# Performance work log

Measured on AMD Instinct MI355X. Metric: run time of the kernel, lower is better.

## Reference

```python
import jax, jax.numpy as jnp
import numpy as np

B, H, W, C = 32, 256, 256, 3
FLAT = (H // 4) * (W // 4) * 64  # 64*64*64 = 262144 after two stride-2 SAME convs


def _conv(x, k, b, stride):
    y = jax.lax.conv_general_dilated(
        x, k, (stride, stride), 'SAME',
        dimension_numbers=('NHWC', 'HWIO', 'NHWC'))
    return jax.nn.relu(y + b)


def _grid_sample(img, theta):
    # STN: build normalized affine grid from theta [B,2,3], bilinear sample with
    # zero padding for out-of-bounds (GridSampler2D semantics).
    b, h, w, c = img.shape
    xs = (2.0 * jnp.arange(w, dtype=img.dtype) + 1.0) / w - 1.0
    ys = (2.0 * jnp.arange(h, dtype=img.dtype) + 1.0) / h - 1.0
    X, Y = jnp.meshgrid(xs, ys)                      # [H,W]
    base = jnp.stack([X, Y, jnp.ones_like(X)], -1)   # [H,W,3]
    g = jnp.einsum('bij,hwj->bhwi', theta, base)     # [B,H,W,2] (x,y) in [-1,1]
    px = (g[..., 0] + 1.0) * 0.5 * w - 0.5
    py = (g[..., 1] + 1.0) * 0.5 * h - 0.5
    x0 = jnp.floor(px); y0 = jnp.floor(py)
    wx1 = px - x0; wx0 = 1.0 - wx1
    wy1 = py - y0; wy0 = 1.0 - wy1

    bidx = jnp.arange(b)[:, None, None]

    def gather(yi, xi):
        valid = (xi >= 0) & (xi < w) & (yi >= 0) & (yi < h)
        xc = jnp.clip(xi, 0, w - 1).astype(jnp.int32)
        yc = jnp.clip(yi, 0, h - 1).astype(jnp.int32)
        v = img[bidx, yc, xc]                        # [B,H,W,C]
        return v * valid[..., None].astype(img.dtype)

    out = (gather(y0, x0) * (wy0 * wx0)[..., None]
           + gather(y0, x0 + 1) * (wy0 * wx1)[..., None]
           + gather(y0 + 1, x0) * (wy1 * wx0)[..., None]
           + gather(y0 + 1, x0 + 1) * (wy1 * wx1)[..., None])
    return out


def setup_inputs() -> dict:
    key = jax.random.key(0)
    ks = jax.random.split(key, 9)
    s = 0.05
    return {
        'inputs': jax.random.uniform(ks[0], (B, H, W, C), jnp.float32),
        'k1': jax.random.normal(ks[1], (3, 3, C, 32), jnp.float32) * s,
        'b1': jnp.zeros((32,), jnp.float32),
        'k2': jax.random.normal(ks[2], (3, 3, 32, 64), jnp.float32) * s,
        'b2': jnp.zeros((64,), jnp.float32),
        'w1': jax.random.normal(ks[3], (FLAT, 128), jnp.float32) * 0.002,
        'd1': jnp.zeros((128,), jnp.float32),
        'w2': jax.random.normal(ks[4], (128, 6), jnp.float32) * s,
        'd2': jnp.asarray([1, 0, 0, 0, 1, 0], jnp.float32),  # identity-ish bias
    }


def reference(inputs, k1, b1, k2, b2, w1, d1, w2, d2):
    x = _conv(inputs, k1, b1, 2)          # [B,H/2,W/2,32]
    x = _conv(x, k2, b2, 2)               # [B,H/4,W/4,64]
    x = x.reshape(x.shape[0], -1)         # [B,FLAT]
    x = jax.nn.relu(x @ w1 + d1)          # [B,128]
    theta = (x @ w2 + d2).reshape(-1, 2, 3)
    return _grid_sample(inputs, theta)
```

## Files before the change

kernel.cpp:

```cpp
#include <hip/hip_runtime.h>

#define IN_H 256
#define IN_W 256
#define C0   3
#define C1   32
#define H1   128
#define C2   64
#define H2   64
#define NB   32
#define K_FLAT (H2*H2*C2)
#define NHID 128

#define A1_IDX(b,y,p,ci,x2) (((((size_t)(b)*H1 + (y))*2 + (p))*C1 + (ci))*64 + (x2))

__global__ __launch_bounds__(256)
void conv1_k(const float* __restrict__ in, const float* __restrict__ k1,
             const float* __restrict__ b1, float* __restrict__ a1p) {
  const int tid = threadIdx.x;
  const int ox  = tid & 127;
  const int cg  = __builtin_amdgcn_readfirstlane((tid >> 7) * 16);
  const int oy  = blockIdx.x;
  const int b   = blockIdx.y;

  float acc[16];
#pragma unroll
  for (int co = 0; co < 16; ++co) acc[co] = b1[cg + co];

#pragma unroll
  for (int dy = 0; dy < 3; ++dy) {
    const int iy  = 2*oy + dy;
    const bool rok = iy < IN_H;
    const int iyc = rok ? iy : (IN_H-1);
#pragma unroll
    for (int dx = 0; dx < 3; ++dx) {
      const int ix  = 2*ox + dx;
      const bool ok = rok && (ix < IN_W);
      const int ixc = (ix < IN_W) ? ix : (IN_W-1);
      const float* ip = in + ((size_t)(b*IN_H + iyc)*IN_W + ixc)*C0;
      const float v0 = ok ? ip[0] : 0.f;
      const float v1 = ok ? ip[1] : 0.f;
      const float v2 = ok ? ip[2] : 0.f;
      const float* wp = k1 + (size_t)((dy*3+dx)*C0)*C1 + cg;
#pragma unroll
      for (int co = 0; co < 16; ++co)
        acc[co] = fmaf(v0, wp[co],
                  fmaf(v1, wp[C1+co],
                  fmaf(v2, wp[2*C1+co], acc[co])));
    }
  }
  const int p  = ox & 1;
  const int x2 = ox >> 1;
#pragma unroll
  for (int co = 0; co < 16; ++co)
    a1p[A1_IDX(b, oy, p, cg + co, x2)] = fmaxf(acc[co], 0.f);
}

__global__ __launch_bounds__(256)
void conv2_k(const float* __restrict__ a1p, const float* __restrict__ k2,
             const float* __restrict__ b2, float* __restrict__ a2) {
  const int tid = threadIdx.x;
  const int ox  = tid & 63;
  const int cg16 = __builtin_amdgcn_readfirstlane((tid >> 6) * 16);
  const int oy  = blockIdx.x;
  const int b   = blockIdx.y;

  float acc[16];
#pragma unroll
  for (int co = 0; co < 16; ++co) acc[co] = b2[cg16 + co];

#pragma unroll
  for (int dy = 0; dy < 3; ++dy) {
    const int iy  = 2*oy + dy;
    const bool rok = iy < H1;
    const int iyc = rok ? iy : (H1-1);
#pragma unroll
    for (int dx = 0; dx < 3; ++dx) {
      const int p   = dx & 1;
      const int x2  = ox + (dx >> 1);
      const bool ok = rok && (x2 < 64);
      const int x2c = (x2 < 64) ? x2 : 63;
      const float* ip = a1p + A1_IDX(b, iyc, p, 0, x2c);
      const float* wp = k2 + (size_t)((dy*3+dx)*C1)*C2 + cg16;
#pragma unroll
      for (int ci = 0; ci < C1; ++ci) {
        float v = ip[(size_t)ci*64];
        v = ok ? v : 0.f;
        const float* wr = wp + (size_t)ci*C2;
#pragma unroll
        for (int co = 0; co < 16; ++co) acc[co] = fmaf(v, wr[co], acc[co]);
      }
    }
  }
  float* op = a2 + ((size_t)(b*H2 + oy)*H2 + ox)*C2 + cg16;
#pragma unroll
  for (int g = 0; g < 4; ++g) {
    float4 o;
    o.x = fmaxf(acc[4*g+0], 0.f);
    o.y = fmaxf(acc[4*g+1], 0.f);
    o.z = fmaxf(acc[4*g+2], 0.f);
    o.w = fmaxf(acc[4*g+3], 0.f);
    ((float4*)op)[g] = o;
  }
}

#define FC1_G   1024
#define KSPAN   (K_FLAT / FC1_G)

__global__ __launch_bounds__(256)
void fc1_partial_k(const float* __restrict__ a2, const float* __restrict__ w1,
                   float* __restrict__ partial) {
  __shared__ __align__(16) float xT[KSPAN*36];
  const int tid = threadIdx.x;
  const int q   = tid & 31;
  const int bo  = tid >> 5;
  const int k0  = blockIdx.x * KSPAN;

  {
    const int lb  = tid >> 3;
    const int lkq = tid & 7;
#pragma unroll
    for (int j = 0; j < 8; ++j) {
      const int k4 = lkq*4 + j*32;
      float4 t = *(const float4*)(a2 + (size_t)lb*K_FLAT + k0 + k4);
      xT[(k4+0)*36 + lb] = t.x;
      xT[(k4+1)*36 + lb] = t.y;
      xT[(k4+2)*36 + lb] = t.z;
      xT[(k4+3)*36 + lb] = t.w;
    }
  }
  __syncthreads();

  float4 a0 = make_float4(0.f,0.f,0.f,0.f), a1v = a0, a2v = a0, a3v = a0;
#pragma unroll 4
  for (int k = 0; k < KSPAN; ++k) {
    const float4 w4 = *(const float4*)(w1 + (size_t)(k0 + k)*NHID + 4*q);
    const float4 xb = *(const float4*)&xT[k*36 + 4*bo];
    a0.x = fmaf(xb.x, w4.x, a0.x); a0.y = fmaf(xb.x, w4.y, a0.y);
    a0.z = fmaf(xb.x, w4.z, a0.z); a0.w = fmaf(xb.x, w4.w, a0.w);
    a1v.x = fmaf(xb.y, w4.x, a1v.x); a1v.y = fmaf(xb.y, w4.y, a1v.y);
    a1v.z = fmaf(xb.y, w4.z, a1v.z); a1v.w = fmaf(xb.y, w4.w, a1v.w);
    a2v.x = fmaf(xb.z, w4.x, a2v.x); a2v.y = fmaf(xb.z, w4.y, a2v.y);
    a2v.z = fmaf(xb.z, w4.z, a2v.z); a2v.w = fmaf(xb.z, w4.w, a2v.w);
    a3v.x = fmaf(xb.w, w4.x, a3v.x); a3v.y = fmaf(xb.w, w4.y, a3v.y);
    a3v.z = fmaf(xb.w, w4.z, a3v.z); a3v.w = fmaf(xb.w, w4.w, a3v.w);
  }

  float* pp = partial + (size_t)blockIdx.x*(NB*NHID) + 4*q;
  *(float4*)(pp + (4*bo+0)*NHID) = a0;
  *(float4*)(pp + (4*bo+1)*NHID) = a1v;
  *(float4*)(pp + (4*bo+2)*NHID) = a2v;
  *(float4*)(pp + (4*bo+3)*NHID) = a3v;
}

__global__ __launch_bounds__(128)
void fc1_reduce1_k(const float* __restrict__ partial, float* __restrict__ partial2) {
  const int t  = blockIdx.x*128 + threadIdx.x;
  const int gc = blockIdx.y;
  float s = 0.f;
#pragma unroll 8
  for (int g = gc*128; g < gc*128+128; ++g) s += partial[(size_t)g*(NB*NHID) + t];
  partial2[(size_t)gc*(NB*NHID) + t] = s;
}

__global__ __launch_bounds__(256)
void fc1_reduce2_k(const float* __restrict__ partial2, const float* __restrict__ d1,
                   float* __restrict__ h) {
  const int t = blockIdx.x*256 + threadIdx.x;
  float s = 0.f;
#pragma unroll
  for (int gc = 0; gc < 8; ++gc) s += partial2[(size_t)gc*(NB*NHID) + t];
  h[t] = fmaxf(s + d1[t & (NHID-1)], 0.f);
}

__global__ __launch_bounds__(192)
void theta_k(const float* __restrict__ h, const float* __restrict__ w2,
             const float* __restrict__ d2, float* __restrict__ theta) {
  const int t = threadIdx.x;
  if (t >= NB*6) return;
  const int b = t / 6, j = t % 6;
  float s0 = 0.f, s1 = 0.f, s2 = 0.f, s3 = 0.f;
  for (int n = 0; n < NHID; n += 4) {
    s0 = fmaf(h[b*NHID + n+0], w2[(n+0)*6 + j], s0);
    s1 = fmaf(h[b*NHID + n+1], w2[(n+1)*6 + j], s1);
    s2 = fmaf(h[b*NHID + n+2], w2[(n+2)*6 + j], s2);
    s3 = fmaf(h[b*NHID + n+3], w2[(n+3)*6 + j], s3);
  }
  theta[t] = (s0 + s1) + (s2 + s3) + d2[j];
}

__global__ __launch_bounds__(256)
void sample_k(const float* __restrict__ img, const float* __restrict__ theta,
              float* __restrict__ out) {
  const int x = threadIdx.x;
  const int y = blockIdx.x & (IN_H-1);
  const int b = blockIdx.x >> 8;
  const float* tp = theta + b*6;
  const float t0 = tp[0], t1 = tp[1], t2 = tp[2];
  const float t3 = tp[3], t4 = tp[4], t5 = tp[5];

  const float xs = (2.f*x + 1.f)*(1.f/IN_W) - 1.f;
  const float ys = (2.f*y + 1.f)*(1.f/IN_H) - 1.f;
  const float gx = fmaf(t0, xs, fmaf(t1, ys, t2));
  const float gy = fmaf(t3, xs, fmaf(t4, ys, t5));
  const float px = fmaf(gx + 1.f, 0.5f*IN_W, -0.5f);
  const float py = fmaf(gy + 1.f, 0.5f*IN_H, -0.5f);

  const float x0f = floorf(px), y0f = floorf(py);
  const int ix0 = (int)x0f, iy0 = (int)y0f;
  const float wx1 = px - x0f, wx0 = 1.f - wx1;
  const float wy1 = py - y0f, wy0 = 1.f - wy1;

  float r = 0.f, g = 0.f, bl = 0.f;
  const float* ib = img + (size_t)b*IN_H*IN_W*C0;

  auto tap = [&](int yi, int xi, float w) {
    const bool v = (xi >= 0) && (xi < IN_W) && (yi >= 0) && (yi < IN_H);
    const int xc = xi < 0 ? 0 : (xi > IN_W-1 ? IN_W-1 : xi);
    const int yc = yi < 0 ? 0 : (yi > IN_H-1 ? IN_H-1 : yi);
    const float* p = ib + ((size_t)yc*IN_W + xc)*C0;
    if (v) {
      r  = fmaf(w, p[0], r);
      g  = fmaf(w, p[1], g);
      bl = fmaf(w, p[2], bl);
    }
  };
  tap(iy0,   ix0,   wy0*wx0);
  tap(iy0,   ix0+1, wy0*wx1);
  tap(iy0+1, ix0,   wy1*wx0);
  tap(iy0+1, ix0+1, wy1*wx1);

  float* op = out + ((size_t)(b*IN_H + y)*IN_W + x)*C0;
  op[0] = r; op[1] = g; op[2] = bl;
}

extern "C" void kernel_launch(void* const* d_in, const int* in_sizes, int n_in,
                              void* d_out, int out_size, void* d_ws, size_t ws_size,
                              hipStream_t stream) {
  const float* in = (const float*)d_in[0];
  const float* k1 = (const float*)d_in[1];
  const float* b1 = (const float*)d_in[2];
  const float* k2 = (const float*)d_in[3];
  const float* b2 = (const float*)d_in[4];
  const float* w1 = (const float*)d_in[5];
  const float* d1 = (const float*)d_in[6];
  const float* w2 = (const float*)d_in[7];
  const float* d2 = (const float*)d_in[8];
  float* out = (float*)d_out;
  float* ws  = (float*)d_ws;

  float* a1p     = ws;
  float* a2      = ws + (size_t)16777216;
  float* partial = ws;
  float* part2   = ws + (size_t)4194304;
  float* h       = ws + (size_t)4227072;
  float* th      = ws + (size_t)4231168;

  hipLaunchKernelGGL(conv1_k,       dim3(128, 32), dim3(256), 0, stream, in, k1, b1, a1p);
  hipLaunchKernelGGL(conv2_k,       dim3(64, 32),  dim3(256), 0, stream, a1p, k2, b2, a2);
  hipLaunchKernelGGL(fc1_partial_k, dim3(FC1_G),   dim3(256), 0, stream, a2, w1, partial);
  hipLaunchKernelGGL(fc1_reduce1_k, dim3(32, 8),   dim3(128), 0, stream, partial, part2);
  hipLaunchKernelGGL(fc1_reduce2_k, dim3(16),      dim3(256), 0, stream, part2, d1, h);
  hipLaunchKernelGGL(theta_k,       dim3(1),       dim3(192), 0, stream, h, w2, d2, th);
  hipLaunchKernelGGL(sample_k,      dim3(NB*IN_H), dim3(256), 0, stream, in, th, out);
}
```

Baseline: 424.6 us.

## Reorder conv1 output layout by parity plane and restructure conv2 loops

```diff
diff --git a/kernel.cpp b/kernel.cpp
--- a/kernel.cpp
+++ b/kernel.cpp
@@ -11,7 +11,7 @@
 #define K_FLAT (H2*H2*C2)
 #define NHID 128
 
-#define A1_IDX(b,y,p,ci,x2) (((((size_t)(b)*H1 + (y))*2 + (p))*C1 + (ci))*64 + (x2))
+#define A1_IDX(b,p,y,ci,x2) ((((((size_t)(b)*2 + (p))*H1 + (y))*C1 + (ci))*64) + (x2))
 
 __global__ __launch_bounds__(256)
 void conv1_k(const float* __restrict__ in, const float* __restrict__ k1,
@@ -29,17 +29,17 @@
 #pragma unroll
   for (int dy = 0; dy < 3; ++dy) {
     const int iy  = 2*oy + dy;
-    const bool rok = iy < IN_H;
-    const int iyc = rok ? iy : (IN_H-1);
+    if (iy >= IN_H) continue;
 #pragma unroll
     for (int dx = 0; dx < 3; ++dx) {
       const int ix  = 2*ox + dx;
-      const bool ok = rok && (ix < IN_W);
-      const int ixc = (ix < IN_W) ? ix : (IN_W-1);
-      const float* ip = in + ((size_t)(b*IN_H + iyc)*IN_W + ixc)*C0;
-      const float v0 = ok ? ip[0] : 0.f;
-      const float v1 = ok ? ip[1] : 0.f;
-      const float v2 = ok ? ip[2] : 0.f;
+      const bool ok = ix < IN_W;
+      const int ixc = ok ? ix : (IN_W-1);
+      const float* ip = in + ((size_t)(b*IN_H + iy)*IN_W + ixc)*C0;
+      const float m  = ok ? 1.f : 0.f;
+      const float v0 = ip[0] * m;
+      const float v1 = ip[1] * m;
+      const float v2 = ip[2] * m;
       const float* wp = k1 + (size_t)((dy*3+dx)*C0)*C1 + cg;
 #pragma unroll
       for (int co = 0; co < 16; ++co)
@@ -52,7 +52,7 @@
   const int x2 = ox >> 1;
 #pragma unroll
   for (int co = 0; co < 16; ++co)
-    a1p[A1_IDX(b, oy, p, cg + co, x2)] = fmaxf(acc[co], 0.f);
+    a1p[A1_IDX(b, p, oy, cg + co, x2)] = fmaxf(acc[co], 0.f);
 }
 
 __global__ __launch_bounds__(256)
@@ -68,27 +68,28 @@
 #pragma unroll
   for (int co = 0; co < 16; ++co) acc[co] = b2[cg16 + co];
 
+  const float xm = (ox == 63) ? 0.f : 1.f;
+
 #pragma unroll
   for (int dy = 0; dy < 3; ++dy) {
-    const int iy  = 2*oy + dy;
-    const bool rok = iy < H1;
-    const int iyc = rok ? iy : (H1-1);
-#pragma unroll
-    for (int dx = 0; dx < 3; ++dx) {
-      const int p   = dx & 1;
-      const int x2  = ox + (dx >> 1);
-      const bool ok = rok && (x2 < 64);
-      const int x2c = (x2 < 64) ? x2 : 63;
-      const float* ip = a1p + A1_IDX(b, iyc, p, 0, x2c);
-      const float* wp = k2 + (size_t)((dy*3+dx)*C1)*C2 + cg16;
-#pragma unroll
-      for (int ci = 0; ci < C1; ++ci) {
-        float v = ip[(size_t)ci*64];
-        v = ok ? v : 0.f;
-        const float* wr = wp + (size_t)ci*C2;
-#pragma unroll
-        for (int co = 0; co < 16; ++co) acc[co] = fmaf(v, wr[co], acc[co]);
-      }
+    const int iy = 2*oy + dy;
+    if (iy >= H1) continue;
+    const float* r0 = a1p + A1_IDX(b, 0, iy, 0, 0) + ox;
+    const float* r1 = a1p + A1_IDX(b, 1, iy, 0, 0) + ox;
+    const float* wp = k2 + (size_t)(dy*3*C1)*C2 + cg16;
+#pragma unroll 4
+    for (int ci = 0; ci < C1; ++ci) {
+      const float v0 = r0[(size_t)ci*64];
+      const float v1 = r1[(size_t)ci*64];
+      const float v2 = r0[(size_t)ci*64 + 1] * xm;
+      const float* w0 = wp + (size_t)ci*C2;
+      const float* w1r = wp + (size_t)(C1 + ci)*C2;
+      const float* w2r = wp + (size_t)(2*C1 + ci)*C2;
+#pragma unroll
+      for (int co = 0; co < 16; ++co)
+        acc[co] = fmaf(v0, w0[co],
+                  fmaf(v1, w1r[co],
+                  fmaf(v2, w2r[co], acc[co])));
     }
   }
   float* op = a2 + ((size_t)(b*H2 + oy)*H2 + ox)*C2 + cg16;
@@ -131,7 +132,7 @@
   __syncthreads();
 
   float4 a0 = make_float4(0.f,0.f,0.f,0.f), a1v = a0, a2v = a0, a3v = a0;
-#pragma unroll 4
+#pragma unroll 8
   for (int k = 0; k < KSPAN; ++k) {
     const float4 w4 = *(const float4*)(w1 + (size_t)(k0 + k)*NHID + 4*q);
     const float4 xb = *(const float4*)&xT[k*36 + 4*bo];
```

Result: faster. 389.0 us (-8.4%).
